# Kernel tuning notes

Hardware: AMD Instinct MI355X
Metric: run time of the kernel (lower is better)

The kernel has to match this reference:

```python
import jax, jax.numpy as jnp
import numpy as np

BN_EPS = 1e-5


def setup_inputs() -> dict:
    key = jax.random.key(0)
    k1, k2, k3, k4 = jax.random.split(key, 4)
    N_IN, N_OUT, K, M, C_IN, C_OUT = 500000, 125000, 27, 60000, 64, 64
    x = jax.random.normal(k1, (N_IN, C_IN), dtype=jnp.float32)
    # Per-offset conv weights, fan-in scaled like Minkowski's kaiming init
    W = jax.random.normal(k2, (K, C_IN, C_OUT), dtype=jnp.float32) * (1.0 / np.sqrt(K * C_IN))
    gamma = jnp.ones((C_OUT,), dtype=jnp.float32)
    beta = jnp.zeros((C_OUT,), dtype=jnp.float32)
    # Kernel map: for each of the 27 offsets, M (input_idx, output_idx) pairs
    in_idx = jax.random.randint(k3, (K, M), 0, N_IN, dtype=jnp.int64)
    out_idx = jax.random.randint(k4, (K, M), 0, N_OUT, dtype=jnp.int64)
    return {"x": x, "W": W, "gamma": gamma, "beta": beta,
            "in_idx": in_idx, "out_idx": out_idx, "n_out": 125000}


def reference(x, W, gamma, beta, in_idx, out_idx, n_out):
    # Sparse 3D conv via kernel map: gather -> per-offset GEMM -> scatter-add.
    C_out = W.shape[-1]
    gathered = x[in_idx]                                   # [K, M, C_in]
    contrib = jnp.einsum('kmc,kcd->kmd', gathered, W)      # [K, M, C_out]
    out = jnp.zeros((n_out, C_out), dtype=x.dtype)
    out = out.at[out_idx.reshape(-1)].add(contrib.reshape(-1, C_out))  # [N_out, C_out]
    # MinkowskiBatchNorm (training mode): per-channel batch stats over all points
    mean = jnp.mean(out, axis=0)
    var = jnp.mean(jnp.square(out - mean), axis=0)         # biased variance
    y = (out - mean) * jax.lax.rsqrt(var + BN_EPS) * gamma + beta
    return y
```

## Files before the change

kernel.cpp:

```cpp
#include <hip/hip_runtime.h>

typedef __attribute__((ext_vector_type(8))) short short8;
typedef __attribute__((ext_vector_type(4))) float f32x4;

#define K_OFF    27
#define M_PAIRS  60000
#define C_DIM    64
#define N_IN     500000
#define N_OUT_C  125000
#define BN_EPS   1e-5f
#define E_TOT    (K_OFF * M_PAIRS)

#define TILES_PER_K  ((M_PAIRS + 63) / 64)
#define TOTAL_WT     (K_OFF * TILES_PER_K)

#define CONTRIB_BYTES ((size_t)E_TOT * C_DIM * 2)
#define WT_OFF    CONTRIB_BYTES
#define WT_BYTES  ((size_t)K_OFF * C_DIM * C_DIM * 2)
#define CNT_OFF   (WT_OFF + WT_BYTES)
#define CNT_BYTES ((size_t)N_OUT_C * 4)
#define OFF_OFF   (CNT_OFF + CNT_BYTES)
#define CUR_OFF   (OFF_OFF + CNT_BYTES)
#define BSUM_OFF  (CUR_OFF + CNT_BYTES)
#define ST_OFF    (BSUM_OFF + 4096)
#define XB_OFF    ((ST_OFF + 512 + 255) & ~(size_t)255)
#define XB_BYTES  ((size_t)N_IN * C_DIM * 2)
#define WS_MID    XB_OFF
#define WS_FULL   (XB_OFF + XB_BYTES)

#define SCAN_BS 256
#define SCAN_NB ((N_OUT_C + SCAN_BS - 1) / SCAN_BS)

__device__ __forceinline__ unsigned short f32_to_bf16(float f) {
    unsigned u = __float_as_uint(f);
    u += 0x7FFFu + ((u >> 16) & 1u);
    return (unsigned short)(u >> 16);
}
__device__ __forceinline__ float bf16f(unsigned short u) {
    return __uint_as_float((unsigned)u << 16);
}

__global__ __launch_bounds__(256) void conv_x(const float* __restrict__ x,
                                              unsigned short* __restrict__ xb) {
    const int tid = blockIdx.x * blockDim.x + threadIdx.x;
    const int T   = gridDim.x * blockDim.x;
    const int n4  = N_IN * C_DIM / 4;
    const float4* x4 = (const float4*)x;
    ushort4* b4 = (ushort4*)xb;
    for (int i = tid; i < n4; i += T) {
        float4 v = x4[i];
        ushort4 o;
        o.x = f32_to_bf16(v.x); o.y = f32_to_bf16(v.y);
        o.z = f32_to_bf16(v.z); o.w = f32_to_bf16(v.w);
        b4[i] = o;
    }
}

__global__ __launch_bounds__(256) void conv_w2(const float* __restrict__ W,
                                               unsigned short* __restrict__ wt) {
    const int tid = blockIdx.x * blockDim.x + threadIdx.x;
    if (tid >= K_OFF * C_DIM * C_DIM) return;
    const int c = tid & 63;
    const int d = (tid >> 6) & 63;
    const int k = tid >> 12;
    wt[tid] = f32_to_bf16(W[(k << 12) + (c << 6) + d]);
}

__global__ __launch_bounds__(256) void hist_k(const int* __restrict__ out_idx,
                                              unsigned* __restrict__ cnt) {
    for (int e = blockIdx.x * blockDim.x + threadIdx.x; e < E_TOT;
         e += gridDim.x * blockDim.x)
        atomicAdd(&cnt[out_idx[e]], 1u);
}

__global__ __launch_bounds__(SCAN_BS) void scan_a(const unsigned* __restrict__ cnt,
                                                  unsigned* __restrict__ off,
                                                  unsigned* __restrict__ bsum) {
    __shared__ unsigned s[SCAN_BS];
    const int idx = blockIdx.x * SCAN_BS + threadIdx.x;
    const unsigned v = (idx < N_OUT_C) ? cnt[idx] : 0u;
    s[threadIdx.x] = v;
    __syncthreads();
    for (int d = 1; d < SCAN_BS; d <<= 1) {
        unsigned t = (threadIdx.x >= d) ? s[threadIdx.x - d] : 0u;
        __syncthreads();
        s[threadIdx.x] += t;
        __syncthreads();
    }
    if (idx < N_OUT_C) off[idx] = s[threadIdx.x] - v;
    if (threadIdx.x == SCAN_BS - 1) bsum[blockIdx.x] = s[threadIdx.x];
}

__global__ __launch_bounds__(512) void scan_b(unsigned* __restrict__ bsum) {
    __shared__ unsigned s[512];
    const unsigned v = (threadIdx.x < SCAN_NB) ? bsum[threadIdx.x] : 0u;
    s[threadIdx.x] = v;
    __syncthreads();
    for (int d = 1; d < 512; d <<= 1) {
        unsigned t = (threadIdx.x >= d) ? s[threadIdx.x - d] : 0u;
        __syncthreads();
        s[threadIdx.x] += t;
        __syncthreads();
    }
    if (threadIdx.x < SCAN_NB) bsum[threadIdx.x] = s[threadIdx.x] - v;
}

__global__ __launch_bounds__(SCAN_BS) void scan_c(unsigned* __restrict__ off,
                                                  unsigned* __restrict__ cur,
                                                  const unsigned* __restrict__ bsum) {
    const int idx = blockIdx.x * SCAN_BS + threadIdx.x;
    if (idx < N_OUT_C) {
        const unsigned o = off[idx] + bsum[blockIdx.x];
        off[idx] = o;
        cur[idx] = o;
    }
}

template<bool BF16G>
__global__ __launch_bounds__(256, 4) void mfma_contrib(
    const float* __restrict__ x, const unsigned short* __restrict__ xb,
    const unsigned short* __restrict__ wt,
    const int* __restrict__ in_idx, const int* __restrict__ out_idx,
    unsigned* __restrict__ cursor, unsigned short* __restrict__ contrib)
{
    const int gwave = blockIdx.x * 4 + (threadIdx.x >> 6);
    if (gwave >= TOTAL_WT) return;
    const int lane = threadIdx.x & 63;
    const int lg = lane >> 4;
    const int lr = lane & 15;

    const int k  = gwave / TILES_PER_K;
    const int t  = gwave % TILES_PER_K;
    const int m0 = t * 64;
    const int kbase = k * M_PAIRS;

    short8 bfr[2][4];
    const unsigned short* wtk = wt + (size_t)k * C_DIM * C_DIM;
#pragma unroll
    for (int ks = 0; ks < 2; ++ks)
#pragma unroll
        for (int ct = 0; ct < 4; ++ct)
            bfr[ks][ct] = *(const short8*)(wtk + (ct * 16 + lr) * C_DIM + ks * 32 + lg * 8);

    int pos = -1;
    {
        const int mrow = m0 + lane;
        if (mrow < M_PAIRS) {
            const int o = out_idx[kbase + mrow];
            pos = (int)atomicAdd(&cursor[o], 1u);
        }
    }

    int aidx[4];
#pragma unroll
    for (int rt = 0; rt < 4; ++rt) {
        const int m = m0 + rt * 16 + lr;
        aidx[rt] = (m < M_PAIRS) ? in_idx[kbase + m] : -1;
    }

    f32x4 acc[4][4] = {};
#pragma unroll
    for (int ks = 0; ks < 2; ++ks) {
#pragma unroll
        for (int rt = 0; rt < 4; ++rt) {
            short8 a = {};
            if (aidx[rt] >= 0) {
                if constexpr (BF16G) {
                    a = *(const short8*)(xb + (size_t)aidx[rt] * C_DIM + ks * 32 + lg * 8);
                } else {
                    const float* xr = x + (size_t)aidx[rt] * C_DIM + ks * 32 + lg * 8;
                    float4 f0 = *(const float4*)xr;
                    float4 f1 = *(const float4*)(xr + 4);
                    a[0] = (short)f32_to_bf16(f0.x); a[1] = (short)f32_to_bf16(f0.y);
                    a[2] = (short)f32_to_bf16(f0.z); a[3] = (short)f32_to_bf16(f0.w);
                    a[4] = (short)f32_to_bf16(f1.x); a[5] = (short)f32_to_bf16(f1.y);
                    a[6] = (short)f32_to_bf16(f1.z); a[7] = (short)f32_to_bf16(f1.w);
                }
            }
#pragma unroll
            for (int ct = 0; ct < 4; ++ct)
                acc[rt][ct] = __builtin_amdgcn_mfma_f32_16x16x32_bf16(
                    a, bfr[ks][ct], acc[rt][ct], 0, 0, 0);
        }
    }

#pragma unroll
    for (int rt = 0; rt < 4; ++rt) {
#pragma unroll
        for (int j = 0; j < 4; ++j) {
            const int r = rt * 16 + lg * 4 + j;
            const int p = __shfl(pos, r);
#pragma unroll
            for (int ct = 0; ct < 4; ++ct) {
                const float v0 = acc[rt][ct][j];
                const float v1 = __shfl_xor(v0, 1);
                if (((lane & 1) == 0) && p >= 0) {
                    const unsigned pk = (unsigned)f32_to_bf16(v0)
                                      | ((unsigned)f32_to_bf16(v1) << 16);
                    *(unsigned*)(contrib + (size_t)p * C_DIM + ct * 16 + lr) = pk;
                }
            }
        }
    }
}

__global__ __launch_bounds__(256) void reduce_bn(
    const unsigned short* __restrict__ contrib, const unsigned* __restrict__ off,
    const unsigned* __restrict__ cnt, float* __restrict__ out,
    float* __restrict__ stats)
{
    __shared__ float ls[128];
    if (threadIdx.x < 128) ls[threadIdx.x] = 0.f;
    __syncthreads();
    const int lane = threadIdx.x & 63;
    const int wv   = threadIdx.x >> 6;
    const int GW   = gridDim.x * 4;
    float ssum = 0.f, ssq = 0.f;
    for (int o = blockIdx.x * 4 + wv; o < N_OUT_C; o += GW) {
        const unsigned base = off[o];
        const unsigned n    = cnt[o];
        const unsigned short* p = contrib + (size_t)base * C_DIM + lane;
        float a0 = 0.f, a1 = 0.f, a2 = 0.f, a3 = 0.f;
        unsigned i = 0;
        for (; i + 4 <= n; i += 4) {
            a0 += bf16f(p[(size_t)(i + 0) * C_DIM]);
            a1 += bf16f(p[(size_t)(i + 1) * C_DIM]);
            a2 += bf16f(p[(size_t)(i + 2) * C_DIM]);
            a3 += bf16f(p[(size_t)(i + 3) * C_DIM]);
        }
        for (; i < n; ++i) a0 += bf16f(p[(size_t)i * C_DIM]);
        const float acc = (a0 + a1) + (a2 + a3);
        out[(size_t)o * C_DIM + lane] = acc;
        ssum += acc;
        ssq = fmaf(acc, acc, ssq);
    }
    atomicAdd(&ls[lane], ssum);
    atomicAdd(&ls[64 + lane], ssq);
    __syncthreads();
    if (threadIdx.x < 128) unsafeAtomicAdd(&stats[threadIdx.x], ls[threadIdx.x]);
}

__global__ __launch_bounds__(256) void bn_apply_f32(
    float* __restrict__ out, const float* __restrict__ stats,
    const float* __restrict__ gamma, const float* __restrict__ beta)
{
    __shared__ float ssc[C_DIM], ssh[C_DIM];
    if (threadIdx.x < C_DIM) {
        const float inv_n = 1.0f / (float)N_OUT_C;
        float mean = stats[threadIdx.x] * inv_n;
        float var  = stats[C_DIM + threadIdx.x] * inv_n - mean * mean;
        float inv  = rsqrtf(var + BN_EPS);
        float s    = inv * gamma[threadIdx.x];
        ssc[threadIdx.x] = s;
        ssh[threadIdx.x] = beta[threadIdx.x] - mean * s;
    }
    __syncthreads();
    const int tid = blockIdx.x * blockDim.x + threadIdx.x;
    const int T   = gridDim.x * blockDim.x;
    const int cq  = (tid & 15) * 4;
    const int total4 = N_OUT_C * C_DIM / 4;
    const float4 sc = make_float4(ssc[cq], ssc[cq+1], ssc[cq+2], ssc[cq+3]);
    const float4 sh = make_float4(ssh[cq], ssh[cq+1], ssh[cq+2], ssh[cq+3]);
    float4* o4 = (float4*)out;
    for (int i = tid; i < total4; i += T) {
        float4 v = o4[i];
        v.x = fmaf(v.x, sc.x, sh.x);
        v.y = fmaf(v.y, sc.y, sh.y);
        v.z = fmaf(v.z, sc.z, sh.z);
        v.w = fmaf(v.w, sc.w, sh.w);
        o4[i] = v;
    }
}

#define FCHUNKS  37
#define FWPK     (FCHUNKS * 4)
#define FSPAN    ((M_PAIRS + FWPK - 1) / FWPK)

__global__ __launch_bounds__(256, 4) void conv_scatter(
    const float* __restrict__ x, const float* __restrict__ W,
    const int* __restrict__ in_idx, const int* __restrict__ out_idx,
    float* __restrict__ out)
{
    const int k     = blockIdx.x / FCHUNKS;
    const int chunk = blockIdx.x % FCHUNKS;
    const int wid   = chunk * 4 + (threadIdx.x >> 6);
    const int lane  = threadIdx.x & 63;
    float wcol[C_DIM];
    const float* Wk = W + (size_t)k * C_DIM * C_DIM;
#pragma unroll
    for (int c = 0; c < C_DIM; ++c) wcol[c] = Wk[c * C_DIM + lane];
    const int kbase = k * M_PAIRS;
    const int m0 = wid * FSPAN;
    const int m1 = (m0 + FSPAN < M_PAIRS) ? m0 + FSPAN : M_PAIRS;
    for (int m = m0; m < m1; ++m) {
        int ii = __builtin_amdgcn_readfirstlane(in_idx[kbase + m]);
        int oi = __builtin_amdgcn_readfirstlane(out_idx[kbase + m]);
        const float* xr = x + (size_t)ii * C_DIM;
        float a0=0.f,a1=0.f,a2=0.f,a3=0.f;
#pragma unroll
        for (int c = 0; c < C_DIM; c += 4) {
            a0 = fmaf(xr[c+0], wcol[c+0], a0);
            a1 = fmaf(xr[c+1], wcol[c+1], a1);
            a2 = fmaf(xr[c+2], wcol[c+2], a2);
            a3 = fmaf(xr[c+3], wcol[c+3], a3);
        }
        unsafeAtomicAdd(out + (size_t)oi * C_DIM + lane, (a0+a1)+(a2+a3));
    }
}

__global__ __launch_bounds__(256) void bn_stats_f32(
    const float* __restrict__ acc, float* __restrict__ stats)
{
    const int tid = blockIdx.x * blockDim.x + threadIdx.x;
    const int T   = gridDim.x * blockDim.x;
    const int cq  = (tid & 15) * 4;
    const int total4 = N_OUT_C * C_DIM / 4;
    float s0=0,s1=0,s2=0,s3=0,q0=0,q1=0,q2=0,q3=0;
    const float4* a4 = (const float4*)acc;
    for (int i = tid; i < total4; i += T) {
        float4 v = a4[i];
        s0+=v.x; q0=fmaf(v.x,v.x,q0);
        s1+=v.y; q1=fmaf(v.y,v.y,q1);
        s2+=v.z; q2=fmaf(v.z,v.z,q2);
        s3+=v.w; q3=fmaf(v.w,v.w,q3);
    }
    __shared__ float ls[128];
    if (threadIdx.x < 128) ls[threadIdx.x] = 0.f;
    __syncthreads();
    atomicAdd(&ls[cq+0],s0); atomicAdd(&ls[cq+1],s1);
    atomicAdd(&ls[cq+2],s2); atomicAdd(&ls[cq+3],s3);
    atomicAdd(&ls[64+cq+0],q0); atomicAdd(&ls[64+cq+1],q1);
    atomicAdd(&ls[64+cq+2],q2); atomicAdd(&ls[64+cq+3],q3);
    __syncthreads();
    if (threadIdx.x < 128) unsafeAtomicAdd(&stats[threadIdx.x], ls[threadIdx.x]);
}

extern "C" void kernel_launch(void* const* d_in, const int* in_sizes, int n_in,
                              void* d_out, int out_size, void* d_ws, size_t ws_size,
                              hipStream_t stream)
{
    const float* x       = (const float*)d_in[0];
    const float* W       = (const float*)d_in[1];
    const float* gamma   = (const float*)d_in[2];
    const float* beta    = (const float*)d_in[3];
    const int*   in_idx  = (const int*)d_in[4];
    const int*   out_idx = (const int*)d_in[5];
    float* out = (float*)d_out;

    if (ws_size >= WS_MID) {
        unsigned short* contrib = (unsigned short*)d_ws;
        unsigned short* wt      = (unsigned short*)((char*)d_ws + WT_OFF);
        unsigned* cnt           = (unsigned*)((char*)d_ws + CNT_OFF);
        unsigned* off           = (unsigned*)((char*)d_ws + OFF_OFF);
        unsigned* cur           = (unsigned*)((char*)d_ws + CUR_OFF);
        unsigned* bsum          = (unsigned*)((char*)d_ws + BSUM_OFF);
        float* stats            = (float*)((char*)d_ws + ST_OFF);
        unsigned short* xb      = (unsigned short*)((char*)d_ws + XB_OFF);
        const bool full         = (ws_size >= WS_FULL);

        hipMemsetAsync(cnt, 0, CNT_BYTES, stream);
        hipMemsetAsync(stats, 0, 128 * sizeof(float), stream);
        conv_w2<<<(K_OFF * C_DIM * C_DIM + 255) / 256, 256, 0, stream>>>(W, wt);
        if (full) conv_x<<<2048, 256, 0, stream>>>(x, xb);
        hist_k<<<2048, 256, 0, stream>>>(out_idx, cnt);
        scan_a<<<SCAN_NB, SCAN_BS, 0, stream>>>(cnt, off, bsum);
        scan_b<<<1, 512, 0, stream>>>(bsum);
        scan_c<<<SCAN_NB, SCAN_BS, 0, stream>>>(off, cur, bsum);
        if (full)
            mfma_contrib<true><<<(TOTAL_WT + 3) / 4, 256, 0, stream>>>(
                x, xb, wt, in_idx, out_idx, cur, contrib);
        else
            mfma_contrib<false><<<(TOTAL_WT + 3) / 4, 256, 0, stream>>>(
                x, xb, wt, in_idx, out_idx, cur, contrib);
        reduce_bn<<<2048, 256, 0, stream>>>(contrib, off, cnt, out, stats);
        bn_apply_f32<<<1024, 256, 0, stream>>>(out, stats, gamma, beta);
    } else {
        float* stats = (float*)d_ws;
        hipMemsetAsync(out, 0, (size_t)N_OUT_C * C_DIM * sizeof(float), stream);
        hipMemsetAsync(stats, 0, 128 * sizeof(float), stream);
        conv_scatter<<<K_OFF * FCHUNKS, 256, 0, stream>>>(x, W, in_idx, out_idx, out);
        bn_stats_f32<<<512, 256, 0, stream>>>(out, stats);
        bn_apply_f32<<<1024, 256, 0, stream>>>(out, stats, gamma, beta);
    }
}
```

Baseline: 394.5 us.

## Merge prep kernels, halve MFMA tile rows, use contiguous output ranges in reduce

Fuses the x conversion, weight transpose and histogram into one prep launch, with block ranges selecting each role. The MFMA contrib kernel now handles 32-row tiles per wave, relying on M being divisible by 32 to drop bounds checks, and raises the occupancy hint to 5 blocks. Each wave in reduce_bn now walks a contiguous span of output rows instead of a strided set, which improves locality of off, cnt and contrib reads. Smaller tiles mean weight fragments are reloaded per 32 rows instead of per 64, and the higher occupancy hint may cause register spills.

Result: no change. 402.1 us (+1.9%).

```diff
diff --git a/kernel.cpp b/kernel.cpp
--- a/kernel.cpp
+++ b/kernel.cpp
@@ -11,7 +11,8 @@
 #define BN_EPS   1e-5f
 #define E_TOT    (K_OFF * M_PAIRS)
 
-#define TILES_PER_K  ((M_PAIRS + 63) / 64)
+#define TILE_ROWS    32
+#define TILES_PER_K  (M_PAIRS / TILE_ROWS)
 #define TOTAL_WT     (K_OFF * TILES_PER_K)
 
 #define CONTRIB_BYTES ((size_t)E_TOT * C_DIM * 2)
@@ -31,6 +32,10 @@
 #define SCAN_BS 256
 #define SCAN_NB ((N_OUT_C + SCAN_BS - 1) / SCAN_BS)
 
+#define PREP_XBLK 2048
+#define PREP_WBLK ((K_OFF * C_DIM * C_DIM + 255) / 256)
+#define PREP_HBLK 1024
+
 __device__ __forceinline__ unsigned short f32_to_bf16(float f) {
     unsigned u = __float_as_uint(f);
     u += 0x7FFFu + ((u >> 16) & 1u);
@@ -40,36 +45,40 @@
     return __uint_as_float((unsigned)u << 16);
 }
 
-__global__ __launch_bounds__(256) void conv_x(const float* __restrict__ x,
-                                              unsigned short* __restrict__ xb) {
-    const int tid = blockIdx.x * blockDim.x + threadIdx.x;
-    const int T   = gridDim.x * blockDim.x;
-    const int n4  = N_IN * C_DIM / 4;
-    const float4* x4 = (const float4*)x;
-    ushort4* b4 = (ushort4*)xb;
-    for (int i = tid; i < n4; i += T) {
-        float4 v = x4[i];
-        ushort4 o;
-        o.x = f32_to_bf16(v.x); o.y = f32_to_bf16(v.y);
-        o.z = f32_to_bf16(v.z); o.w = f32_to_bf16(v.w);
-        b4[i] = o;
-    }
-}
-
-__global__ __launch_bounds__(256) void conv_w2(const float* __restrict__ W,
-                                               unsigned short* __restrict__ wt) {
-    const int tid = blockIdx.x * blockDim.x + threadIdx.x;
-    if (tid >= K_OFF * C_DIM * C_DIM) return;
-    const int c = tid & 63;
-    const int d = (tid >> 6) & 63;
-    const int k = tid >> 12;
-    wt[tid] = f32_to_bf16(W[(k << 12) + (c << 6) + d]);
-}
-
-__global__ __launch_bounds__(256) void hist_k(const int* __restrict__ out_idx,
-                                              unsigned* __restrict__ cnt) {
-    for (int e = blockIdx.x * blockDim.x + threadIdx.x; e < E_TOT;
-         e += gridDim.x * blockDim.x)
+__global__ __launch_bounds__(256) void prep(
+    const float* __restrict__ x, unsigned short* __restrict__ xb,
+    const float* __restrict__ W, unsigned short* __restrict__ wt,
+    const int* __restrict__ out_idx, unsigned* __restrict__ cnt, int nx)
+{
+    int b = blockIdx.x;
+    if (b < nx) {
+        const int tid = b * 256 + threadIdx.x;
+        const int T   = nx * 256;
+        const int n4  = N_IN * C_DIM / 4;
+        const float4* x4 = (const float4*)x;
+        ushort4* b4 = (ushort4*)xb;
+        for (int i = tid; i < n4; i += T) {
+            float4 v = x4[i];
+            ushort4 o;
+            o.x = f32_to_bf16(v.x); o.y = f32_to_bf16(v.y);
+            o.z = f32_to_bf16(v.z); o.w = f32_to_bf16(v.w);
+            b4[i] = o;
+        }
+        return;
+    }
+    b -= nx;
+    if (b < PREP_WBLK) {
+        const int tid = b * 256 + threadIdx.x;
+        if (tid < K_OFF * C_DIM * C_DIM) {
+            const int c = tid & 63;
+            const int d = (tid >> 6) & 63;
+            const int k = tid >> 12;
+            wt[tid] = f32_to_bf16(W[(k << 12) + (c << 6) + d]);
+        }
+        return;
+    }
+    b -= PREP_WBLK;
+    for (int e = b * 256 + threadIdx.x; e < E_TOT; e += PREP_HBLK * 256)
         atomicAdd(&cnt[out_idx[e]], 1u);
 }
 
@@ -117,7 +126,7 @@
 }
 
 template<bool BF16G>
-__global__ __launch_bounds__(256, 4) void mfma_contrib(
+__global__ __launch_bounds__(256, 5) void mfma_contrib(
     const float* __restrict__ x, const unsigned short* __restrict__ xb,
     const unsigned short* __restrict__ wt,
     const int* __restrict__ in_idx, const int* __restrict__ out_idx,
@@ -131,7 +140,7 @@
 
     const int k  = gwave / TILES_PER_K;
     const int t  = gwave % TILES_PER_K;
-    const int m0 = t * 64;
+    const int m0 = t * TILE_ROWS;
     const int kbase = k * M_PAIRS;
 
     short8 bfr[2][4];
@@ -142,40 +151,31 @@
         for (int ct = 0; ct < 4; ++ct)
             bfr[ks][ct] = *(const short8*)(wtk + (ct * 16 + lr) * C_DIM + ks * 32 + lg * 8);
 
-    int pos = -1;
-    {
-        const int mrow = m0 + lane;
-        if (mrow < M_PAIRS) {
-            const int o = out_idx[kbase + mrow];
-            pos = (int)atomicAdd(&cursor[o], 1u);
-        }
-    }
-
-    int aidx[4];
-#pragma unroll
-    for (int rt = 0; rt < 4; ++rt) {
-        const int m = m0 + rt * 16 + lr;
-        aidx[rt] = (m < M_PAIRS) ? in_idx[kbase + m] : -1;
-    }
-
-    f32x4 acc[4][4] = {};
+    int pos = 0;
+    if (lane < TILE_ROWS)
+        pos = (int)atomicAdd(&cursor[out_idx[kbase + m0 + lane]], 1u);
+
+    int aidx[2];
+#pragma unroll
+    for (int rt = 0; rt < 2; ++rt)
+        aidx[rt] = in_idx[kbase + m0 + rt * 16 + lr];
+
+    f32x4 acc[2][4] = {};
 #pragma unroll
     for (int ks = 0; ks < 2; ++ks) {
 #pragma unroll
-        for (int rt = 0; rt < 4; ++rt) {
-            short8 a = {};
-            if (aidx[rt] >= 0) {
-                if constexpr (BF16G) {
-                    a = *(const short8*)(xb + (size_t)aidx[rt] * C_DIM + ks * 32 + lg * 8);
-                } else {
-                    const float* xr = x + (size_t)aidx[rt] * C_DIM + ks * 32 + lg * 8;
-                    float4 f0 = *(const float4*)xr;
-                    float4 f1 = *(const float4*)(xr + 4);
-                    a[0] = (short)f32_to_bf16(f0.x); a[1] = (short)f32_to_bf16(f0.y);
-                    a[2] = (short)f32_to_bf16(f0.z); a[3] = (short)f32_to_bf16(f0.w);
-                    a[4] = (short)f32_to_bf16(f1.x); a[5] = (short)f32_to_bf16(f1.y);
-                    a[6] = (short)f32_to_bf16(f1.z); a[7] = (short)f32_to_bf16(f1.w);
-                }
+        for (int rt = 0; rt < 2; ++rt) {
+            short8 a;
+            if constexpr (BF16G) {
+                a = *(const short8*)(xb + (size_t)aidx[rt] * C_DIM + ks * 32 + lg * 8);
+            } else {
+                const float* xr = x + (size_t)aidx[rt] * C_DIM + ks * 32 + lg * 8;
+                float4 f0 = *(const float4*)xr;
+                float4 f1 = *(const float4*)(xr + 4);
+                a[0] = (short)f32_to_bf16(f0.x); a[1] = (short)f32_to_bf16(f0.y);
+                a[2] = (short)f32_to_bf16(f0.z); a[3] = (short)f32_to_bf16(f0.w);
+                a[4] = (short)f32_to_bf16(f1.x); a[5] = (short)f32_to_bf16(f1.y);
+                a[6] = (short)f32_to_bf16(f1.z); a[7] = (short)f32_to_bf16(f1.w);
             }
 #pragma unroll
             for (int ct = 0; ct < 4; ++ct)
@@ -185,7 +185,7 @@
     }
 
 #pragma unroll
-    for (int rt = 0; rt < 4; ++rt) {
+    for (int rt = 0; rt < 2; ++rt) {
 #pragma unroll
         for (int j = 0; j < 4; ++j) {
             const int r = rt * 16 + lg * 4 + j;
@@ -194,7 +194,7 @@
             for (int ct = 0; ct < 4; ++ct) {
                 const float v0 = acc[rt][ct][j];
                 const float v1 = __shfl_xor(v0, 1);
-                if (((lane & 1) == 0) && p >= 0) {
+                if ((lane & 1) == 0) {
                     const unsigned pk = (unsigned)f32_to_bf16(v0)
                                       | ((unsigned)f32_to_bf16(v1) << 16);
                     *(unsigned*)(contrib + (size_t)p * C_DIM + ct * 16 + lr) = pk;
@@ -213,10 +213,14 @@
     if (threadIdx.x < 128) ls[threadIdx.x] = 0.f;
     __syncthreads();
     const int lane = threadIdx.x & 63;
-    const int wv   = threadIdx.x >> 6;
-    const int GW   = gridDim.x * 4;
+    const int wid  = blockIdx.x * 4 + (threadIdx.x >> 6);
+    const int NW   = gridDim.x * 4;
+    const int span = (N_OUT_C + NW - 1) / NW;
+    const int o0 = wid * span;
+    const int o1 = (o0 + span < N_OUT_C) ? o0 + span : N_OUT_C;
+
     float ssum = 0.f, ssq = 0.f;
-    for (int o = blockIdx.x * 4 + wv; o < N_OUT_C; o += GW) {
+    for (int o = o0; o < o1; ++o) {
         const unsigned base = off[o];
         const unsigned n    = cnt[o];
         const unsigned short* p = contrib + (size_t)base * C_DIM + lane;
@@ -357,12 +361,12 @@
         float* stats            = (float*)((char*)d_ws + ST_OFF);
         unsigned short* xb      = (unsigned short*)((char*)d_ws + XB_OFF);
         const bool full         = (ws_size >= WS_FULL);
+        const int nx            = full ? PREP_XBLK : 0;
 
         hipMemsetAsync(cnt, 0, CNT_BYTES, stream);
         hipMemsetAsync(stats, 0, 128 * sizeof(float), stream);
-        conv_w2<<<(K_OFF * C_DIM * C_DIM + 255) / 256, 256, 0, stream>>>(W, wt);
-        if (full) conv_x<<<2048, 256, 0, stream>>>(x, xb);
-        hist_k<<<2048, 256, 0, stream>>>(out_idx, cnt);
+        prep<<<nx + PREP_WBLK + PREP_HBLK, 256, 0, stream>>>(
+            x, xb, W, wt, out_idx, cnt, nx);
         scan_a<<<SCAN_NB, SCAN_BS, 0, stream>>>(cnt, off, bsum);
         scan_b<<<1, 512, 0, stream>>>(bsum);
         scan_c<<<SCAN_NB, SCAN_BS, 0, stream>>>(off, cur, bsum);
```
